# Kernel tuning notes

Hardware: AMD Instinct MI355X
Metric: run time of the kernel (lower is better)

## Reference

```python
import math
import jax, jax.numpy as jnp
import numpy as np

EPS = 1e-4
FMAX = 18  # max filtersize for scale clamped to 2.5: ceil(3*2^2.5+0.5)=18 -> kernel 37x37
KSZ = 2 * FMAX + 1


def _conv2d(x, w, b):
    # 3x3 conv, padding 1, NCHW / OIHW (cross-correlation, matches torch)
    y = jax.lax.conv_general_dilated(x, w, (1, 1), [(1, 1), (1, 1)],
                                     dimension_numbers=('NCHW', 'OIHW', 'NCHW'))
    return y + b[None, :, None, None]


def _basis_filters(scale):
    # scale: [B] -> [B,3,K,K] (g, dgdx, dgdy), masked to the per-sample support
    std = 2.0 ** scale                              # [B]
    fs = jnp.ceil(3.0 * std + 0.5)                  # per-sample filtersize
    x = jnp.arange(-FMAX, FMAX + 1, dtype=jnp.float32)          # [K]
    m = (jnp.abs(x)[None, :] <= fs[:, None]).astype(jnp.float32)  # [B,K] support mask
    e = jnp.exp(-0.5 * (x[None, :] / std[:, None]) ** 2) * m      # masked 1D gaussian [B,K]
    g = e[:, :, None] * e[:, None, :]                              # [B,K,K]
    g = g / jnp.sum(g, axis=(1, 2), keepdims=True)
    c = (-x[None, :] / (std[:, None] ** 3 * 2.0 * math.pi)) * e    # [B,K]
    dgdx = c[:, :, None] * e[:, None, :]   # varies along first spatial dim (x[0])
    dgdx = dgdx / jnp.sum(jnp.abs(dgdx), axis=(1, 2), keepdims=True)
    dgdy = e[:, :, None] * c[:, None, :]   # varies along second spatial dim (x[1])
    dgdy = dgdy / jnp.sum(jnp.abs(dgdy), axis=(1, 2), keepdims=True)
    return jnp.stack([g, dgdx, dgdy], axis=1)  # [B,3,K,K]


def setup_inputs() -> dict:
    key = jax.random.key(0)
    ks = jax.random.split(key, 7)
    B, H, W = 8, 512, 512
    batch = jax.random.uniform(ks[0], (B, 3, H, W), dtype=jnp.float32)
    gcm = jnp.array([[0.06, 0.63, 0.27], [0.3, 0.04, -0.35], [0.34, -0.6, 0.17]],
                    dtype=jnp.float32)
    w1 = jax.random.normal(ks[1], (16, 3, 3, 3), dtype=jnp.float32) * 0.1
    b1 = jax.random.normal(ks[2], (16,), dtype=jnp.float32) * 0.01
    w2 = jax.random.normal(ks[3], (16, 16, 3, 3), dtype=jnp.float32) * 0.1
    b2 = jax.random.normal(ks[4], (16,), dtype=jnp.float32) * 0.01
    w3 = jax.random.normal(ks[5], (1, 16, 3, 3), dtype=jnp.float32) * 0.1
    b3 = jax.random.normal(ks[6], (1,), dtype=jnp.float32) * 0.01
    return {"batch": batch, "gcm": gcm, "w1": w1, "b1": b1,
            "w2": w2, "b2": b2, "w3": w3, "b3": b3}


def reference(batch, gcm, w1, b1, w2, b2, w3, b3):
    B, _, H, W = batch.shape
    # ---- RGB order prior (non-differentiable, no_grad in torch) ----
    oh = lambda i: jax.nn.one_hot(i, 3, axis=1, dtype=batch.dtype)
    mx = jnp.argmax(batch, axis=1)                 # first max
    mn = jnp.argmin(batch, axis=1)
    bf = batch[:, ::-1]
    mx2 = 2 - jnp.argmax(bf, axis=1)               # last max
    mn2 = 2 - jnp.argmin(bf, axis=1)
    RGB_order = jax.lax.stop_gradient(
        0.5 * (oh(mx) + oh(mx2)) - 0.5 * (oh(mn) + oh(mn2)))  # [B,3,H,W]

    # ---- per-sample adaptive scale from small CNN ----
    h = jax.nn.silu(_conv2d(batch, w1, b1))
    h = jax.nn.silu(_conv2d(h, w2, b2))
    s = _conv2d(h, w3, b3)
    scale = jnp.clip(jnp.mean(s, axis=(1, 2, 3)), -2.5, 2.5)   # [B]

    # ---- Gaussian color model ----
    xg = jnp.einsum('ij,bjhw->bihw', gcm, batch)  # [B,3,H,W] -> (E, El, Ell)

    # ---- per-sample Gaussian basis convolution, batched via grouped conv ----
    basis = _basis_filters(scale)                                  # [B,3,K,K]
    xin = xg.reshape(1, B * 3, H, W)
    wk = jnp.broadcast_to(basis[:, None], (B, 3, 3, KSZ, KSZ)).reshape(B * 9, 1, KSZ, KSZ)
    out = jax.lax.conv_general_dilated(xin, wk, (1, 1), [(FMAX, FMAX), (FMAX, FMAX)],
                                       feature_group_count=B * 3,
                                       dimension_numbers=('NCHW', 'OIHW', 'NCHW'))
    out = out.reshape(B, 3, 3, H, W)   # [B, chan(E/El/Ell), filt(g/dx/dy), H, W]
    E = out[:, 0, 0:1]
    Ex = out[:, 0, 1:2]
    Ey = out[:, 0, 2:3]
    El = out[:, 1, 0:1]
    Ell = out[:, 2, 0:1]

    Hf = jnp.arctan(El / (Ell + EPS))
    S = jnp.log((El ** 2 + Ell ** 2) / (E ** 2 + EPS) + EPS)
    Ww = jnp.arctan((Ex / (E + EPS)) ** 2 + (Ey / (E + EPS)) ** 2)
    return jnp.concatenate([Hf, S, RGB_order, Ww], axis=1)  # [B,6,H,W]
```

## Files before the change

kernel.cpp:

```cpp
#include <hip/hip_runtime.h>
#include <hip/hip_bf16.h>

constexpr int BN = 8, HH = 512, WW = 512;
constexpr int PIX = HH * WW;
constexpr float EPSF = 1e-4f;

__device__ __forceinline__ float b2f(__hip_bfloat16 x) { return __bfloat162float(x); }
__device__ __forceinline__ __hip_bfloat16 f2b(float x) { return __float2bfloat16(x); }
__device__ __forceinline__ unsigned short bfbits(float x) {
    union { __hip_bfloat16 b; unsigned short u; } cv; cv.b = f2b(x); return cv.u;
}

typedef __attribute__((ext_vector_type(8))) short bf16x8;
typedef __attribute__((ext_vector_type(4))) float f32x4;

constexpr int OFF_TOT = 0;
constexpr int OFF_ROW0 = 128;
constexpr int OFF_ROW1 = 256;
constexpr int OFF_COL0 = 384;
constexpr int OFF_COL1 = 512;
constexpr int OFF_COR = 640;
constexpr int OFF_WR  = 2048;
constexpr int OFF_EH  = 4608;
constexpr int OFF_CH  = 5120;
constexpr size_t OFF_TPB = 65536;
constexpr size_t TP_BYTES = (size_t)4 * BN * PIX * 4;
constexpr size_t WS_NEEDED = OFF_TPB + TP_BYTES;

__global__ void prep_kernel(const float* __restrict__ w2, float* __restrict__ wsf) {
    int t = threadIdx.x;
    for (int i = t; i < 640; i += 256) wsf[i] = 0.f;
    unsigned short* ab = (unsigned short*)(wsf + OFF_WR);
    for (int idx = t; idx < 5120; idx += 256) {
        int part = idx / 2560;
        int id = idx - part * 2560;
        int ks = id >> 9, rem = id & 511, lane = rem >> 3, j = id & 7;
        int oc = lane & 15, q = lane >> 4;
        int k = q * 8 + j;
        int tap = 2 * ks + (k >> 4), ic = k & 15;
        float val = (tap <= 8) ? w2[oc * 144 + ic * 9 + tap] : 0.f;
        float hv = b2f(f2b(val));
        ab[idx] = (part == 0) ? bfbits(val) : bfbits(val - hv);
    }
}

__device__ __forceinline__ void conv1_px(const float v[27], const float* __restrict__ w1,
                                         const float* __restrict__ b1, unsigned int u[8]) {
    float o[16];
#pragma unroll
    for (int oc = 0; oc < 16; oc++) {
        float a = b1[oc];
#pragma unroll
        for (int j = 0; j < 27; j++) a += v[j] * w1[oc * 27 + j];
        o[oc] = a / (1.f + __expf(-a));
    }
#pragma unroll
    for (int k = 0; k < 8; k++)
        u[k] = (unsigned int)bfbits(o[2 * k]) | ((unsigned int)bfbits(o[2 * k + 1]) << 16);
}

__global__ __launch_bounds__(256) void conv12_kernel(const float* __restrict__ batch,
                                                     const float* __restrict__ w1,
                                                     const float* __restrict__ b1,
                                                     const unsigned short* __restrict__ abuf,
                                                     const float* __restrict__ b2v,
                                                     const float* __restrict__ gcm,
                                                     float* __restrict__ wsf,
                                                     float* __restrict__ out) {
    __shared__ float st[3][12][68];
    __shared__ uint4 h1s[10 * 66 * 2];
    __shared__ float part[4][16];

    int tx = threadIdx.x;
    int lane = tx & 63, wave = tx >> 6;
    int n = lane & 15, q = lane >> 4;
    int w0 = blockIdx.x * 64, h0 = blockIdx.y * 8, b = blockIdx.z;

    union { uint4 u; bf16x8 v; } cv;
    bf16x8 ah[5], al[5];
    const uint4* ab4 = (const uint4*)abuf;
#pragma unroll
    for (int ks = 0; ks < 5; ks++) {
        cv.u = ab4[ks * 64 + lane];       ah[ks] = cv.v;
        cv.u = ab4[320 + ks * 64 + lane]; al[ks] = cv.v;
    }

    const float* pb = batch + (size_t)(b * 3) * PIX;

    for (int i = tx; i < 2448; i += 256) {
        int ch = i / 816;
        int rem = i - ch * 816;
        int r = rem / 68, c = rem - r * 68;
        int gh = h0 - 2 + r, gw = w0 - 2 + c;
        float v = 0.f;
        if (gh >= 0 && gh < HH && gw >= 0 && gw < WW)
            v = pb[(size_t)ch * PIX + (size_t)gh * WW + gw];
        st[ch][r][c] = v;
    }
    __syncthreads();

    for (int i = tx; i < 660; i += 256) {
        int r = i / 66, c = i - r * 66;
        int gh = h0 - 1 + r, gw = w0 - 1 + c;
        unsigned int u[8];
        if (gh >= 0 && gh < HH && gw >= 0 && gw < WW) {
            float v[27];
#pragma unroll
            for (int ic = 0; ic < 3; ic++)
#pragma unroll
                for (int kh = 0; kh < 3; kh++)
#pragma unroll
                    for (int kw = 0; kw < 3; kw++)
                        v[ic * 9 + kh * 3 + kw] = st[ic][r + kh][c + kw];
            conv1_px(v, w1, b1, u);
        } else {
#pragma unroll
            for (int k = 0; k < 8; k++) u[k] = 0u;
        }
        int swz = (c >> 2) & 1;
        int base = i * 2;
        h1s[base + swz]       = make_uint4(u[0], u[1], u[2], u[3]);
        h1s[base + (swz ^ 1)] = make_uint4(u[4], u[5], u[6], u[7]);
    }

    for (int j = tx; j < 512; j += 256) {
        int rr = j >> 6, ccx = j & 63;
        float v0 = st[0][rr + 2][ccx + 2];
        float v1 = st[1][rr + 2][ccx + 2];
        float v2 = st[2][rr + 2][ccx + 2];
        int mx  = (v0 >= v1 && v0 >= v2) ? 0 : ((v1 >= v2) ? 1 : 2);
        int mx2 = (v2 >= v1 && v2 >= v0) ? 2 : ((v1 >= v0) ? 1 : 0);
        int mn  = (v0 <= v1 && v0 <= v2) ? 0 : ((v1 <= v2) ? 1 : 2);
        int mn2 = (v2 <= v1 && v2 <= v0) ? 2 : ((v1 <= v0) ? 1 : 0);
        size_t p = (size_t)(h0 + rr) * WW + (w0 + ccx);
#pragma unroll
        for (int c = 0; c < 3; c++) {
            float r = 0.5f * ((float)(c == mx) + (float)(c == mx2))
                    - 0.5f * ((float)(c == mn) + (float)(c == mn2));
            out[(size_t)(b * 6 + 2 + c) * PIX + p] = r;
        }
    }
    __syncthreads();

    float tt[4] = {0, 0, 0, 0};
    float cs0[4] = {0, 0, 0, 0};
    float cs1[4] = {0, 0, 0, 0};
    for (int rloc = 0; rloc < 2; rloc++) {
        int row = wave * 2 + rloc;
        int grow = h0 + row;
        f32x4 acc[4] = {{0,0,0,0},{0,0,0,0},{0,0,0,0},{0,0,0,0}};
#pragma unroll
        for (int ks = 0; ks < 5; ks++) {
            int tap = 2 * ks + (q >> 1); if (tap > 8) tap = 8;
            int dh = tap / 3 - 1, dw = tap % 3 - 1;
            int half = q & 1;
            int lr = row + 1 + dh;
#pragma unroll
            for (int t = 0; t < 4; t++) {
                int c = 1 + dw + t * 16 + n;
                cv.u = h1s[(lr * 66 + c) * 2 + (half ^ ((c >> 2) & 1))];
                acc[t] = __builtin_amdgcn_mfma_f32_16x16x32_bf16(ah[ks], cv.v, acc[t], 0, 0, 0);
                acc[t] = __builtin_amdgcn_mfma_f32_16x16x32_bf16(al[ks], cv.v, acc[t], 0, 0, 0);
            }
        }
        float sv[4][4];
#pragma unroll
        for (int t = 0; t < 4; t++)
#pragma unroll
            for (int r = 0; r < 4; r++) {
                float a = acc[t][r] + b2v[q * 4 + r];
                sv[t][r] = a / (1.f + __expf(-a));
            }
#pragma unroll
        for (int r = 0; r < 4; r++) tt[r] += sv[0][r] + sv[1][r] + sv[2][r] + sv[3][r];
        if (grow == 0 || grow == HH - 1) {
            int off = (grow == 0) ? OFF_ROW0 : OFF_ROW1;
#pragma unroll
            for (int r = 0; r < 4; r++) {
                float x = sv[0][r] + sv[1][r] + sv[2][r] + sv[3][r];
#pragma unroll
                for (int d = 1; d < 16; d <<= 1) x += __shfl_xor(x, d, 64);
                if (n == 0) atomicAdd(&wsf[off + b * 16 + q * 4 + r], x);
            }
        }
        if (blockIdx.x == 0 && n == 0)
#pragma unroll
            for (int r = 0; r < 4; r++) cs0[r] += sv[0][r];
        if (blockIdx.x == 7 && n == 15)
#pragma unroll
            for (int r = 0; r < 4; r++) cs1[r] += sv[3][r];
        if ((grow == 0 || grow == HH - 1)) {
            int hi = (grow == 0) ? 0 : 1;
            if (blockIdx.x == 0 && n == 0)
#pragma unroll
                for (int r = 0; r < 4; r++)
                    wsf[OFF_COR + ((b * 2 + hi) * 2 + 0) * 16 + q * 4 + r] = sv[0][r];
            if (blockIdx.x == 7 && n == 15)
#pragma unroll
                for (int r = 0; r < 4; r++)
                    wsf[OFF_COR + ((b * 2 + hi) * 2 + 1) * 16 + q * 4 + r] = sv[3][r];
        }
    }
    if (blockIdx.x == 0 && n == 0)
#pragma unroll
        for (int r = 0; r < 4; r++) atomicAdd(&wsf[OFF_COL0 + b * 16 + q * 4 + r], cs0[r]);
    if (blockIdx.x == 7 && n == 15)
#pragma unroll
        for (int r = 0; r < 4; r++) atomicAdd(&wsf[OFF_COL1 + b * 16 + q * 4 + r], cs1[r]);
#pragma unroll
    for (int r = 0; r < 4; r++) {
        float x = tt[r];
#pragma unroll
        for (int d = 1; d < 16; d <<= 1) x += __shfl_xor(x, d, 64);
        tt[r] = x;
    }
    if (n == 0)
#pragma unroll
        for (int r = 0; r < 4; r++) part[wave][q * 4 + r] = tt[r];
    __syncthreads();
    if (tx < 16)
        atomicAdd(&wsf[OFF_TOT + b * 16 + tx],
                  part[0][tx] + part[1][tx] + part[2][tx] + part[3][tx]);
}

__global__ void filter_kernel(const float* __restrict__ w3, const float* __restrict__ b3,
                              float* __restrict__ wsf) {
    int b = blockIdx.x, t = threadIdx.x;
    __shared__ float red[160];
    float val = 0.f;
    if (t < 144) {
        int ic = t / 9, tap = t % 9, kh = tap / 3, kw = tap % 3;
        float T = wsf[OFF_TOT + b * 16 + ic];
        int hi = -1, wi = -1;
        if (kh == 0) { T -= wsf[OFF_ROW1 + b * 16 + ic]; hi = 1; }
        else if (kh == 2) { T -= wsf[OFF_ROW0 + b * 16 + ic]; hi = 0; }
        if (kw == 0) { T -= wsf[OFF_COL1 + b * 16 + ic]; wi = 1; }
        else if (kw == 2) { T -= wsf[OFF_COL0 + b * 16 + ic]; wi = 0; }
        if (hi >= 0 && wi >= 0) T += wsf[OFF_COR + ((b * 2 + hi) * 2 + wi) * 16 + ic];
        val = w3[t] * T;
    }
    red[t] = val;
    __syncthreads();
    __shared__ float sh_mean;
    if (t == 0) {
        float S = 0.f;
        for (int i = 0; i < 144; i++) S += red[i];
        sh_mean = b3[0] + S * (1.f / (float)PIX);
    }
    __syncthreads();
    float scale = fminf(2.5f, fmaxf(-2.5f, sh_mean));
    float sd = exp2f(scale);
    float fs = ceilf(3.f * sd + 0.5f);
    float e = 0.f, c = 0.f;
    if (t < 37) {
        float x = (float)(t - 18);
        if (fabsf(x) <= fs) {
            float qq = x / sd;
            e = __expf(-0.5f * qq * qq);
            c = -x / (sd * sd * sd * 6.28318530717958647692f) * e;
        }
    }
    __shared__ float sa[40], sb[40];
    if (t < 37) { sa[t] = e; sb[t] = fabsf(c); }
    __syncthreads();
    __shared__ float Se, Sc;
    if (t == 0) {
        float a = 0.f, d = 0.f;
        for (int i = 0; i < 37; i++) { a += sa[i]; d += sb[i]; }
        Se = a; Sc = d;
    }
    __syncthreads();
    if (t < 37) {
        wsf[OFF_EH + b * 37 + t] = e / Se;
        wsf[OFF_CH + b * 37 + t] = c / Sc;
    }
}

__device__ __forceinline__ int skw(int c) { return c + (c >> 5); }
__global__ __launch_bounds__(256, 4) void horiz_kernel(const float* __restrict__ batch,
                                                       const float* __restrict__ gcm,
                                                       const float* __restrict__ ehat,
                                                       const float* __restrict__ chat,
                                                       float* __restrict__ t) {
    __shared__ float xr[2][3][566];
    int tx = threadIdx.x;
    int h0 = blockIdx.x * 2;
    int b  = blockIdx.y;
    const float* pb = batch + (size_t)(b * 3) * PIX;
    float g0 = gcm[0], g1 = gcm[1], g2 = gcm[2];
    float g3 = gcm[3], g4 = gcm[4], g5 = gcm[5];
    float g6 = gcm[6], g7 = gcm[7], g8 = gcm[8];
    for (int i = tx; i < 2 * 548; i += 256) {
        int r = i / 548, c = i - r * 548;
        int gw = c - 18;
        float v0 = 0.f, v1 = 0.f, v2 = 0.f;
        if (gw >= 0 && gw < WW) {
            size_t p = (size_t)(h0 + r) * WW + gw;
            v0 = pb[p]; v1 = pb[(size_t)PIX + p]; v2 = pb[2 * (size_t)PIX + p];
        }
        int cs = skw(c);
        xr[r][0][cs] = g0 * v0 + g1 * v1 + g2 * v2;
        xr[r][1][cs] = g3 * v0 + g4 * v1 + g5 * v2;
        xr[r][2][cs] = g6 * v0 + g7 * v1 + g8 * v2;
    }
    __syncthreads();
    int r = tx >> 7, colbase = (tx & 127) * 4;
    const float* eh = ehat + b * 37; const float* ch = chat + b * 37;
    float a0[4] = {}, a1[4] = {}, a2[4] = {}, a3[4] = {};
#pragma unroll 4
    for (int kk = 0; kk < 40; kk++) {
        int cs = skw(colbase + kk);
        float x0 = xr[r][0][cs], x1 = xr[r][1][cs], x2 = xr[r][2][cs];
#pragma unroll
        for (int i = 0; i < 4; i++) {
            int k = kk - i;
            if (k >= 0 && k < 37) {
                float ce = eh[k], cc = ch[k];
                a0[i] += ce * x0; a1[i] += ce * x1;
                a2[i] += ce * x2; a3[i] += cc * x0;
            }
        }
    }
    const size_t PL = (size_t)BN * PIX;
    size_t p = (size_t)b * PIX + (size_t)(h0 + r) * WW + colbase;
    *(float4*)&t[0 * PL + p] = make_float4(a0[0], a0[1], a0[2], a0[3]);
    *(float4*)&t[1 * PL + p] = make_float4(a1[0], a1[1], a1[2], a1[3]);
    *(float4*)&t[2 * PL + p] = make_float4(a2[0], a2[1], a2[2], a2[3]);
    *(float4*)&t[3 * PL + p] = make_float4(a3[0], a3[1], a3[2], a3[3]);
}

__global__ __launch_bounds__(256, 4) void vert_kernel(const float* __restrict__ t,
                                                      const float* __restrict__ ehat,
                                                      const float* __restrict__ chat,
                                                      float* __restrict__ out) {
    int tx = threadIdx.x;
    int j = blockIdx.x * 64 + (tx & 63);
    int r0 = (blockIdx.y * 4 + (tx >> 6)) * 4;
    int b = blockIdx.z;
    const float* eh = ehat + b * 37; const float* ch = chat + b * 37;
    const size_t PL = (size_t)BN * PIX;
    const float* t0 = t + (size_t)b * PIX;
    float E[4] = {}, Ex[4] = {}, Ey[4] = {}, El[4] = {}, Ell[4] = {};
#pragma unroll 4
    for (int kk = 0; kk < 40; kk++) {
        int gr = r0 - 18 + kk;
        if (gr >= 0 && gr < HH) {
            size_t idx = (size_t)gr * WW + j;
            float v0 = t0[idx], v1 = t0[PL + idx], v2 = t0[2 * PL + idx], v3 = t0[3 * PL + idx];
#pragma unroll
            for (int i = 0; i < 4; i++) {
                int k = kk - i;
                if (k >= 0 && k < 37) {
                    float ce = eh[k], cc = ch[k];
                    E[i] += ce * v0; Ex[i] += cc * v0; Ey[i] += ce * v3;
                    El[i] += ce * v1; Ell[i] += ce * v2;
                }
            }
        }
    }
#pragma unroll
    for (int i = 0; i < 4; i++) {
        int h = r0 + i;
        float Hf = atanf(El[i] / (Ell[i] + EPSF));
        float S = logf((El[i] * El[i] + Ell[i] * Ell[i]) / (E[i] * E[i] + EPSF) + EPSF);
        float rx = Ex[i] / (E[i] + EPSF), ry = Ey[i] / (E[i] + EPSF);
        float Wv = atanf(rx * rx + ry * ry);
        size_t base = (size_t)(b * 6) * PIX + (size_t)h * WW + j;
        out[base] = Hf;
        out[base + PIX] = S;
        out[base + 5 * (size_t)PIX] = Wv;
    }
}

extern "C" void kernel_launch(void* const* d_in, const int* in_sizes, int n_in,
                              void* d_out, int out_size, void* d_ws, size_t ws_size,
                              hipStream_t stream) {
    const float* batch = (const float*)d_in[0];
    const float* gcm   = (const float*)d_in[1];
    const float* w1    = (const float*)d_in[2];
    const float* b1    = (const float*)d_in[3];
    const float* w2    = (const float*)d_in[4];
    const float* b2    = (const float*)d_in[5];
    const float* w3    = (const float*)d_in[6];
    const float* b3    = (const float*)d_in[7];
    float* out = (float*)d_out;

    if (ws_size < WS_NEEDED) return;

    float* wsf = (float*)d_ws;
    float* tpl = (float*)((char*)d_ws + OFF_TPB);
    float* ehat = wsf + OFF_EH;
    float* chat = wsf + OFF_CH;

    prep_kernel<<<dim3(1), dim3(256), 0, stream>>>(w2, wsf);
    conv12_kernel<<<dim3(8, 64, 8), dim3(256), 0, stream>>>(
        batch, w1, b1, (const unsigned short*)(wsf + OFF_WR), b2, gcm, wsf, out);
    filter_kernel<<<dim3(8), dim3(160), 0, stream>>>(w3, b3, wsf);
    horiz_kernel<<<dim3(256, 8), dim3(256), 0, stream>>>(batch, gcm, ehat, chat, tpl);
    vert_kernel<<<dim3(8, 32, 8), dim3(256), 0, stream>>>(tpl, ehat, chat, out);
}
```

Baseline: 272.8 us.

## Move first 3x3 conv onto bf16 MFMA with split-precision weights

The scalar per-pixel 27x16 FMA loop for conv1 is replaced by MFMA 16x16x32 bf16 instructions. Weights are pre-split into high and low bf16 parts in the prep kernel, and the input taps are gathered via precomputed LDS offsets. SiLU now uses a reciprocal intrinsic and packed bf16 conversion, and the conv2 weight and bias loads are deferred until after the first phase to ease register pressure. Inputs are rounded to bf16, so conv1 precision is lower than the fp32 path it replaces.

```diff
diff --git a/kernel.cpp b/kernel.cpp
--- a/kernel.cpp
+++ b/kernel.cpp
@@ -9,6 +9,14 @@
 __device__ __forceinline__ __hip_bfloat16 f2b(float x) { return __float2bfloat16(x); }
 __device__ __forceinline__ unsigned short bfbits(float x) {
     union { __hip_bfloat16 b; unsigned short u; } cv; cv.b = f2b(x); return cv.u;
+}
+__device__ __forceinline__ unsigned int cvtpk(float lo, float hi) {
+    unsigned int r;
+    asm("v_cvt_pk_bf16_f32 %0, %1, %2" : "=v"(r) : "v"(lo), "v"(hi));
+    return r;
+}
+__device__ __forceinline__ float silu(float a) {
+    return a * __builtin_amdgcn_rcpf(1.f + __expf(-a));
 }
 
 typedef __attribute__((ext_vector_type(8))) short bf16x8;
@@ -20,6 +28,7 @@
 constexpr int OFF_COL0 = 384;
 constexpr int OFF_COL1 = 512;
 constexpr int OFF_COR = 640;
+constexpr int OFF_W1R = 1280;
 constexpr int OFF_WR  = 2048;
 constexpr int OFF_EH  = 4608;
 constexpr int OFF_CH  = 5120;
@@ -27,7 +36,8 @@
 constexpr size_t TP_BYTES = (size_t)4 * BN * PIX * 4;
 constexpr size_t WS_NEEDED = OFF_TPB + TP_BYTES;
 
-__global__ void prep_kernel(const float* __restrict__ w2, float* __restrict__ wsf) {
+__global__ void prep_kernel(const float* __restrict__ w1, const float* __restrict__ w2,
+                            float* __restrict__ wsf) {
     int t = threadIdx.x;
     for (int i = t; i < 640; i += 256) wsf[i] = 0.f;
     unsigned short* ab = (unsigned short*)(wsf + OFF_WR);
@@ -42,29 +52,24 @@
         float hv = b2f(f2b(val));
         ab[idx] = (part == 0) ? bfbits(val) : bfbits(val - hv);
     }
-}
-
-__device__ __forceinline__ void conv1_px(const float v[27], const float* __restrict__ w1,
-                                         const float* __restrict__ b1, unsigned int u[8]) {
-    float o[16];
-#pragma unroll
-    for (int oc = 0; oc < 16; oc++) {
-        float a = b1[oc];
-#pragma unroll
-        for (int j = 0; j < 27; j++) a += v[j] * w1[oc * 27 + j];
-        o[oc] = a / (1.f + __expf(-a));
-    }
-#pragma unroll
-    for (int k = 0; k < 8; k++)
-        u[k] = (unsigned int)bfbits(o[2 * k]) | ((unsigned int)bfbits(o[2 * k + 1]) << 16);
+    unsigned short* a1 = (unsigned short*)(wsf + OFF_W1R);
+    for (int idx = t; idx < 1024; idx += 256) {
+        int part = idx >> 9;
+        int id = idx & 511;
+        int lane = id >> 3, j = id & 7;
+        int oc = lane & 15, q = lane >> 4;
+        int k = q * 8 + j;
+        float val = (k < 27) ? w1[oc * 27 + k] : 0.f;
+        float hv = b2f(f2b(val));
+        a1[idx] = (part == 0) ? bfbits(val) : bfbits(val - hv);
+    }
 }
 
 __global__ __launch_bounds__(256) void conv12_kernel(const float* __restrict__ batch,
-                                                     const float* __restrict__ w1,
+                                                     const unsigned short* __restrict__ w1buf,
                                                      const float* __restrict__ b1,
                                                      const unsigned short* __restrict__ abuf,
                                                      const float* __restrict__ b2v,
-                                                     const float* __restrict__ gcm,
                                                      float* __restrict__ wsf,
                                                      float* __restrict__ out) {
     __shared__ float st[3][12][68];
@@ -77,14 +82,6 @@
     int w0 = blockIdx.x * 64, h0 = blockIdx.y * 8, b = blockIdx.z;
 
     union { uint4 u; bf16x8 v; } cv;
-    bf16x8 ah[5], al[5];
-    const uint4* ab4 = (const uint4*)abuf;
-#pragma unroll
-    for (int ks = 0; ks < 5; ks++) {
-        cv.u = ab4[ks * 64 + lane];       ah[ks] = cv.v;
-        cv.u = ab4[320 + ks * 64 + lane]; al[ks] = cv.v;
-    }
-
     const float* pb = batch + (size_t)(b * 3) * PIX;
 
     for (int i = tx; i < 2448; i += 256) {
@@ -97,30 +94,53 @@
             v = pb[(size_t)ch * PIX + (size_t)gh * WW + gw];
         st[ch][r][c] = v;
     }
-    __syncthreads();
-
-    for (int i = tx; i < 660; i += 256) {
+
+    bf16x8 w1h, w1l;
+    const uint4* w14 = (const uint4*)w1buf;
+    cv.u = w14[lane];      w1h = cv.v;
+    cv.u = w14[64 + lane]; w1l = cv.v;
+    int koff[8];
+#pragma unroll
+    for (int j = 0; j < 8; j++) {
+        int k = q * 8 + j;
+        int kk = (k < 27) ? k : 0;
+        int ic = kk / 9, rem = kk - ic * 9, kh = rem / 3, kw = rem - kh * 3;
+        koff[j] = ic * 816 + kh * 68 + kw;
+    }
+    float b1q[4];
+#pragma unroll
+    for (int r = 0; r < 4; r++) b1q[r] = b1[q * 4 + r];
+    bool hiq = (q == 3);
+    __syncthreads();
+
+    const float* stf = &st[0][0][0];
+    unsigned int* hw = (unsigned int*)h1s;
+    for (int g = wave; g < 42; g += 4) {
+        int i = g * 16 + n; if (i > 659) i = 659;
         int r = i / 66, c = i - r * 66;
+        int base = r * 68 + c;
+        float x[8];
+#pragma unroll
+        for (int j = 0; j < 8; j++) x[j] = stf[base + koff[j]];
+#pragma unroll
+        for (int j = 3; j < 8; j++) x[j] = hiq ? 0.f : x[j];
+        union { unsigned int w[4]; bf16x8 v; } bb;
+        bb.w[0] = cvtpk(x[0], x[1]);
+        bb.w[1] = cvtpk(x[2], x[3]);
+        bb.w[2] = cvtpk(x[4], x[5]);
+        bb.w[3] = cvtpk(x[6], x[7]);
+        f32x4 a = {0, 0, 0, 0};
+        a = __builtin_amdgcn_mfma_f32_16x16x32_bf16(w1h, bb.v, a, 0, 0, 0);
+        a = __builtin_amdgcn_mfma_f32_16x16x32_bf16(w1l, bb.v, a, 0, 0, 0);
         int gh = h0 - 1 + r, gw = w0 - 1 + c;
-        unsigned int u[8];
-        if (gh >= 0 && gh < HH && gw >= 0 && gw < WW) {
-            float v[27];
-#pragma unroll
-            for (int ic = 0; ic < 3; ic++)
-#pragma unroll
-                for (int kh = 0; kh < 3; kh++)
-#pragma unroll
-                    for (int kw = 0; kw < 3; kw++)
-                        v[ic * 9 + kh * 3 + kw] = st[ic][r + kh][c + kw];
-            conv1_px(v, w1, b1, u);
-        } else {
-#pragma unroll
-            for (int k = 0; k < 8; k++) u[k] = 0u;
-        }
+        bool ok = ((unsigned)gh < (unsigned)HH) && ((unsigned)gw < (unsigned)WW);
+        unsigned int p0 = cvtpk(silu(a[0] + b1q[0]), silu(a[1] + b1q[1]));
+        unsigned int p1 = cvtpk(silu(a[2] + b1q[2]), silu(a[3] + b1q[3]));
+        p0 = ok ? p0 : 0u;
+        p1 = ok ? p1 : 0u;
         int swz = (c >> 2) & 1;
-        int base = i * 2;
-        h1s[base + swz]       = make_uint4(u[0], u[1], u[2], u[3]);
-        h1s[base + (swz ^ 1)] = make_uint4(u[4], u[5], u[6], u[7]);
+        int slot = i * 2 + ((q >= 2) ? (swz ^ 1) : swz);
+        *(uint2*)&hw[slot * 4 + (q & 1) * 2] = make_uint2(p0, p1);
     }
 
     for (int j = tx; j < 512; j += 256) {
@@ -142,6 +162,17 @@
     }
     __syncthreads();
 
+    bf16x8 ah[5], al[5];
+    const uint4* ab4 = (const uint4*)abuf;
+#pragma unroll
+    for (int ks = 0; ks < 5; ks++) {
+        cv.u = ab4[ks * 64 + lane];       ah[ks] = cv.v;
+        cv.u = ab4[320 + ks * 64 + lane]; al[ks] = cv.v;
+    }
+    float b2q[4];
+#pragma unroll
+    for (int r = 0; r < 4; r++) b2q[r] = b2v[q * 4 + r];
+
     float tt[4] = {0, 0, 0, 0};
     float cs0[4] = {0, 0, 0, 0};
     float cs1[4] = {0, 0, 0, 0};
@@ -167,10 +198,8 @@
 #pragma unroll
         for (int t = 0; t < 4; t++)
 #pragma unroll
-            for (int r = 0; r < 4; r++) {
-                float a = acc[t][r] + b2v[q * 4 + r];
-                sv[t][r] = a / (1.f + __expf(-a));
-            }
+            for (int r = 0; r < 4; r++)
+                sv[t][r] = silu(acc[t][r] + b2q[r]);
 #pragma unroll
         for (int r = 0; r < 4; r++) tt[r] += sv[0][r] + sv[1][r] + sv[2][r] + sv[3][r];
         if (grow == 0 || grow == HH - 1) {
@@ -392,9 +421,10 @@
     float* ehat = wsf + OFF_EH;
     float* chat = wsf + OFF_CH;
 
-    prep_kernel<<<dim3(1), dim3(256), 0, stream>>>(w2, wsf);
+    prep_kernel<<<dim3(1), dim3(256), 0, stream>>>(w1, w2, wsf);
     conv12_kernel<<<dim3(8, 64, 8), dim3(256), 0, stream>>>(
-        batch, w1, b1, (const unsigned short*)(wsf + OFF_WR), b2, gcm, wsf, out);
+        batch, (const unsigned short*)(wsf + OFF_W1R), b1,
+        (const unsigned short*)(wsf + OFF_WR), b2, wsf, out);
     filter_kernel<<<dim3(8), dim3(160), 0, stream>>>(w3, b3, wsf);
     horiz_kernel<<<dim3(256, 8), dim3(256), 0, stream>>>(batch, gcm, ehat, chat, tpl);
     vert_kernel<<<dim3(8, 32, 8), dim3(256), 0, stream>>>(tpl, ehat, chat, out);
```

Result: faster. 251.5 us (-7.8%).
